# Kernel optimization log

Hardware: AMD Instinct MI355X
Metric: run time of the kernel (lower is better)

The kernel has to match this reference:

```python
import jax, jax.numpy as jnp
import numpy as np
import math

B, N, DIM, H, DH = 4, 1024, 512, 8, 64
INNER = H * DH
TEMP = 0.1
REG_LAMBDA = 0.3
LARGE_NEG = -1.0e9


def setup_inputs() -> dict:
    key = jax.random.key(0)
    ks = jax.random.split(key, 10)
    x = jax.random.normal(ks[0], (B, N, DIM), dtype=jnp.float32)
    # binary channel mask with guaranteed self-connection on the diagonal
    m = jax.random.randint(ks[1], (B, N, N), 0, 2, dtype=jnp.int32)
    eye_i = jnp.eye(N, dtype=jnp.int32)[None]
    attn_mask = jnp.maximum(m, eye_i)
    s = 0.02
    Wq = jax.random.normal(ks[2], (DIM, INNER), dtype=jnp.float32) * s
    bq = jnp.zeros((INNER,), dtype=jnp.float32)
    Wk = jax.random.normal(ks[3], (DIM, INNER), dtype=jnp.float32) * s
    bk = jnp.zeros((INNER,), dtype=jnp.float32)
    Wv = jax.random.normal(ks[4], (DIM, INNER), dtype=jnp.float32) * s
    bv = jnp.zeros((INNER,), dtype=jnp.float32)
    Wo = jax.random.normal(ks[5], (INNER, DIM), dtype=jnpp_dummy()) * s if False else jax.random.normal(ks[5], (INNER, DIM), dtype=jnp.float32) * s
    bo = jnp.zeros((DIM,), dtype=jnp.float32)
    return {"x": x, "attn_mask": attn_mask, "Wq": Wq, "bq": bq, "Wk": Wk,
            "bk": bk, "Wv": Wv, "bv": bv, "Wo": Wo, "bo": bo}


def jnp_dummy():
    return jnp.float32


def _split_heads(t):
    # [b, n, h*d] -> [b, h, n, d]
    return t.reshape(t.shape[0], t.shape[1], H, DH).transpose(0, 2, 1, 3)


def _dynamical_contrastive_loss(scores, attn_mask_f, norm_matrix):
    # cosine similarity matrix (scores / |q||k|)
    cos = scores / norm_matrix
    e = jnp.exp(cos / TEMP)                                   # [b,h,n,n]
    pos = (e * attn_mask_f[:, None]).sum(-1)                  # [b,h,n]
    allsum = e.sum(-1)                                        # [b,h,n]
    clustering = -jnp.log(pos / allsum)
    eye = jnp.eye(N, dtype=attn_mask_f.dtype)
    regular = jnp.abs(attn_mask_f - eye[None]).sum((-2, -1)) / (N * (N - 1))
    return clustering.mean() + REG_LAMBDA * regular.mean()


def reference(x, attn_mask, Wq, bq, Wk, bk, Wv, bv, Wo, bo):
    q = _split_heads(x @ Wq + bq)  # [b,h,n,d]
    k = _split_heads(x @ Wk + bk)
    v = _split_heads(x @ Wv + bv)
    scale = 1.0 / math.sqrt(DH)

    scores = jnp.einsum('bhid,bhjd->bhij', q, k)
    q_norm = jnp.linalg.norm(q, axis=-1, keepdims=True)       # [b,h,n,1]
    k_norm = jnp.linalg.norm(k, axis=-1, keepdims=True)
    norm_matrix = q_norm * jnp.swapaxes(k_norm, -1, -2)       # [b,h,n,n]

    am = attn_mask.astype(scores.dtype)[:, None]              # [b,1,n,n]
    masked_scores = scores * am + (1.0 - am) * LARGE_NEG
    # faithful replication of the all-blocked-row special case
    # (-1e9 is finite so this is a no-op unless scores contain -inf)
    row_all_blocked = jnp.all(jnp.isneginf(masked_scores), axis=-1, keepdims=True)
    masked_scores = jnp.where(row_all_blocked, jnp.zeros_like(masked_scores), masked_scores)

    dcl = _dynamical_contrastive_loss(scores, attn_mask.astype(scores.dtype), norm_matrix)

    attn = jax.nn.softmax(masked_scores * scale, axis=-1)
    out = jnp.einsum('bhij,bhjd->bhid', attn, v)
    out = out.transpose(0, 2, 1, 3).reshape(x.shape[0], x.shape[1], INNER)
    # dropout is identity in eval mode
    return out @ Wo + bo, attn, dcl
```

## Files before the change

### kernel.cpp

```cpp
#include <hip/hip_runtime.h>
#include <hip/hip_bf16.h>
#include <math.h>

#define BB 4
#define NTOK 1024
#define DIMD 512
#define HH 8
#define DH 64
#define INNER 512
#define BH (BB*HH)
#define ROWS (BB*NTOK)
#define SCALE 0.125f
#define INV_TEMP 10.0f

typedef __bf16 bf16_t;
using bf16x4 = __attribute__((ext_vector_type(4))) __bf16;
using bf16x8 = __attribute__((ext_vector_type(8))) __bf16;
using f32x4  = __attribute__((ext_vector_type(4))) float;

__device__ __forceinline__ int swz(int row, int e) { return e ^ ((row & 7) << 3); }

__device__ __forceinline__ void gload_lds16(const bf16_t* g, bf16_t* l)
{
    __builtin_amdgcn_global_load_lds(
        (const __attribute__((address_space(1))) void*)g,
        (__attribute__((address_space(3))) void*)l, 16, 0, 0);
}

template<int TM, int TN, int MT, int NT>
__device__ __forceinline__ void gemm_core(
    const bf16_t* __restrict__ A, int ldA,
    const bf16_t* __restrict__ B, int ldB, int K,
    bf16_t* As, bf16_t* Bs, f32x4 (&acc)[MT][NT])
{
    const int t = threadIdx.x;
    const int w = t >> 6, l = t & 63;
    constexpr int WGN = TN / (NT * 16);
    const int wm = w / WGN, wn = w % WGN;
    const int lrow = l & 15, lk = (l >> 4) * 8;

    for (int k0 = 0; k0 < K; k0 += 32) {
        #pragma unroll
        for (int it = 0; it < TM / 64; ++it) {
            int r = (t >> 2) + it * 64;
            gload_lds16(&A[(size_t)r * ldA + k0 + (t & 3) * 8],
                        As + ((size_t)it * 256 + w * 64) * 8);
        }
        #pragma unroll
        for (int it = 0; it < TN / 64; ++it) {
            int r = (t >> 2) + it * 64;
            gload_lds16(&B[(size_t)r * ldB + k0 + (t & 3) * 8],
                        Bs + ((size_t)it * 256 + w * 64) * 8);
        }
        __syncthreads();
        bf16x8 af[MT], bf[NT];
        #pragma unroll
        for (int mt = 0; mt < MT; ++mt)
            af[mt] = *(const bf16x8*)&As[(wm * MT * 16 + mt * 16 + lrow) * 32 + lk];
        #pragma unroll
        for (int nt = 0; nt < NT; ++nt)
            bf[nt] = *(const bf16x8*)&Bs[(wn * NT * 16 + nt * 16 + lrow) * 32 + lk];
        #pragma unroll
        for (int mt = 0; mt < MT; ++mt)
            #pragma unroll
            for (int nt = 0; nt < NT; ++nt)
                acc[mt][nt] = __builtin_amdgcn_mfma_f32_16x16x32_bf16(
                    af[mt], bf[nt], acc[mt][nt], 0, 0, 0);
        __syncthreads();
    }
}

__global__ __launch_bounds__(256) void prep_kernel(
    const float* __restrict__ x,
    const float* __restrict__ Wq, const float* __restrict__ Wk,
    const float* __restrict__ Wv, const float* __restrict__ Wo,
    const int* __restrict__ mask,
    bf16_t* __restrict__ xb, bf16_t* __restrict__ wt,
    unsigned int* __restrict__ mp)
{
    __shared__ float tile[32][33];
    const int bid = blockIdx.x, t = threadIdx.x;
    if (bid < 2048) {
        int idx = bid * 256 + t;
        float4 v = ((const float4*)x)[idx];
        bf16x4 o = { (bf16_t)v.x, (bf16_t)v.y, (bf16_t)v.z, (bf16_t)v.w };
        ((bf16x4*)xb)[idx] = o;
    } else if (bid < 3072) {
        int f = bid - 2048;
        int bx = f & 15, by = (f >> 4) & 15, z = f >> 8;
        const float* src = (z == 0) ? Wq : (z == 1) ? Wk : (z == 2) ? Wv : Wo;
        bf16_t* dst = wt + (size_t)z * DIMD * INNER;
        const int tx = t & 31, ty = t >> 5;
        const int rBase = by * 32, cBase = bx * 32;
        #pragma unroll
        for (int i = 0; i < 4; ++i)
            tile[ty + i * 8][tx] = src[(size_t)(rBase + ty + i * 8) * INNER + cBase + tx];
        __syncthreads();
        #pragma unroll
        for (int i = 0; i < 4; ++i)
            dst[(size_t)(cBase + ty + i * 8) * DIMD + rBase + tx] = (bf16_t)tile[tx][ty + i * 8];
    } else {
        int f = bid - 3072;
        int rr = f & 255, b = f >> 8;
        const int* mb = mask + ((size_t)(b * NTOK + rr * 4)) * NTOK;
        #pragma unroll
        for (int u = 0; u < 4; ++u) {
            int col = u * 256 + t;
            unsigned int o = (unsigned)mb[col]
                           | ((unsigned)mb[NTOK + col] << 8)
                           | ((unsigned)mb[2 * NTOK + col] << 16)
                           | ((unsigned)mb[3 * NTOK + col] << 24);
            mp[((size_t)b * 256 + rr) * NTOK + col] = o;
        }
    }
}

__global__ __launch_bounds__(256) void qkv_gemm(
    const bf16_t* __restrict__ xb, const bf16_t* __restrict__ wt,
    const float* __restrict__ bq, const float* __restrict__ bk,
    const float* __restrict__ bv,
    bf16_t* __restrict__ qb, bf16_t* __restrict__ kb, bf16_t* __restrict__ vt,
    float* __restrict__ iqn, float* __restrict__ ikn)
{
    __shared__ __align__(16) bf16_t As[128 * 32];
    __shared__ __align__(16) bf16_t Bs[128 * 32];
    const int z = blockIdx.z;
    const bf16_t* Bp = wt + (size_t)z * DIMD * INNER;
    const float* bias = (z == 0) ? bq : (z == 1) ? bk : bv;
    const int rowBase = blockIdx.y * 128, colBase = blockIdx.x * 128;

    f32x4 acc[4][4] = {};
    gemm_core<128, 128, 4, 4>(xb + (size_t)rowBase * DIMD, DIMD,
                              Bp + (size_t)colBase * DIMD, DIMD, DIMD,
                              As, Bs, acc);

    const int l = threadIdx.x & 63, w = threadIdx.x >> 6;
    const int wm = w >> 1, wn = w & 1;
    float nsum[4][4] = {};
    #pragma unroll
    for (int mt = 0; mt < 4; ++mt)
        #pragma unroll
        for (int nt = 0; nt < 4; ++nt)
            #pragma unroll
            for (int r = 0; r < 4; ++r) {
                int grow = rowBase + wm * 64 + mt * 16 + (l >> 4) * 4 + r;
                int gcol = colBase + wn * 64 + nt * 16 + (l & 15);
                float val = acc[mt][nt][r] + bias[gcol];
                bf16_t vb16 = (bf16_t)val;
                int b = grow >> 10, n = grow & 1023, h = gcol >> 6, d = gcol & 63;
                if (z == 0)
                    qb[(((size_t)b * HH + h) * NTOK + n) * DH + d] = vb16;
                else if (z == 1)
                    kb[(((size_t)b * HH + h) * NTOK + n) * DH + d] = vb16;
                else
                    vt[(((size_t)b * HH + h) * DH + d) * NTOK + n] = vb16;
                if (z < 2) { float vb = (float)vb16; nsum[mt][r] += vb * vb; }
            }
    if (z < 2) {
        float* dst = (z == 0) ? iqn : ikn;
        const int h = (colBase >> 6) + wn;
        #pragma unroll
        for (int mt = 0; mt < 4; ++mt)
            #pragma unroll
            for (int r = 0; r < 4; ++r) {
                float s = nsum[mt][r];
                s += __shfl_xor(s, 8); s += __shfl_xor(s, 4);
                s += __shfl_xor(s, 2); s += __shfl_xor(s, 1);
                if ((l & 15) == 0) {
                    int grow = rowBase + wm * 64 + mt * 16 + (l >> 4) * 4 + r;
                    int b = grow >> 10, n = grow & 1023;
                    dst[((size_t)b * HH + h) * NTOK + n] = 1.0f / sqrtf(s);
                }
            }
    }
}

__device__ __forceinline__ void stage_k(const bf16_t* K, int col0, bf16_t* Ks, int t)
{
    const int w = t >> 6, l = t & 63;
    #pragma unroll
    for (int u = 0; u < 4; ++u) {
        int g = u * 256 + w * 64 + l;
        int kr = g >> 3, ep = (g & 7) * 8;
        gload_lds16(K + (size_t)(col0 + kr) * DH + (ep ^ ((kr & 7) << 3)),
                    Ks + ((size_t)u * 256 + w * 64) * 8);
    }
}
__device__ __forceinline__ void stage_v(const bf16_t* V, int col0, bf16_t* Vs, int t)
{
    const int w = t >> 6, l = t & 63;
    #pragma unroll
    for (int u = 0; u < 4; ++u) {
        int g = u * 256 + w * 64 + l;
        int d = g >> 4, ep = (g & 15) * 8;
        gload_lds16(V + (size_t)d * NTOK + col0 + (ep ^ ((d & 7) << 3)),
                    Vs + ((size_t)u * 256 + w * 64) * 8);
    }
}

__global__ __launch_bounds__(256) void attn_fused(
    const bf16_t* __restrict__ qb, const bf16_t* __restrict__ kb,
    const bf16_t* __restrict__ vt, const unsigned int* __restrict__ mp,
    const float* __restrict__ iqn, const float* __restrict__ ikn,
    float* __restrict__ attnf, bf16_t* __restrict__ ctxb,
    float* __restrict__ cl, float* __restrict__ rg)
{
    __shared__ __align__(16) bf16_t Ks[128 * 64];
    __shared__ __align__(16) bf16_t Vs[64 * 128];
    __shared__ __align__(16) bf16_t Ps[4 * 16 * 128];
    const int bh = blockIdx.y;
    const int b = bh >> 3, h = bh & 7;
    const int rowBase = blockIdx.x * 64;
    const bf16_t* Q = qb + (size_t)bh * NTOK * DH;
    const bf16_t* K = kb + (size_t)bh * NTOK * DH;
    const bf16_t* V = vt + (size_t)bh * DH * NTOK;
    const float* iknr = ikn + (size_t)bh * NTOK;
    const int t = threadIdx.x, w = t >> 6, l = t & 63;
    const int l15 = l & 15, q = l >> 4;
    bf16_t* Pw = Ps + w * (16 * 128);

    bf16x8 af[2];
    {
        const bf16_t* qrow = Q + (size_t)(rowBase + w * 16 + l15) * DH + q * 8;
        af[0] = *(const bf16x8*)(qrow);
        af[1] = *(const bf16x8*)(qrow + 32);
    }
    const int tok = rowBase + w * 16 + q * 4;
    float iqn4[4];
    #pragma unroll
    for (int r = 0; r < 4; ++r)
        iqn4[r] = iqn[(size_t)bh * NTOK + tok + r];
    const unsigned int* mrow = mp + ((size_t)b * 256 + (tok >> 2)) * NTOK;

    float alls[4] = {}, pos[4] = {}, esum[4] = {}, regf[4] = {};

    for (int ct = 0; ct < 8; ++ct) {
        const int col0 = ct * 128;
        stage_k(K, col0, Ks, t);
        __syncthreads();
        f32x4 sacc[8] = {};
        #pragma unroll
        for (int ks = 0; ks < 2; ++ks) {
            int koff = ks * 32 + q * 8;
            #pragma unroll
            for (int nt = 0; nt < 8; ++nt) {
                int kr = nt * 16 + l15;
                bf16x8 bfk = *(const bf16x8*)&Ks[kr * 64 + swz(kr, koff)];
                sacc[nt] = __builtin_amdgcn_mfma_f32_16x16x32_bf16(af[ks], bfk, sacc[nt], 0, 0, 0);
            }
        }
        #pragma unroll
        for (int nt = 0; nt < 8; ++nt) {
            int c = col0 + nt * 16 + l15;
            float ik = iknr[c];
            unsigned int mm = mrow[c];
            #pragma unroll
            for (int r = 0; r < 4; ++r) {
                float s = sacc[nt][r];
                float mbit = (float)((mm >> (8 * r)) & 1u);
                float e1 = __expf(s * iqn4[r] * ik * INV_TEMP);
                float e2 = __expf(s * SCALE);
                alls[r] += e1;
                pos[r]  += e1 * mbit;
                esum[r] += e2 * mbit;
                regf[r] += mbit;
            }
        }
        __syncthreads();
    }
    float inv4[4];
    #pragma unroll
    for (int r = 0; r < 4; ++r) {
        #pragma unroll
        for (int off = 8; off; off >>= 1) {
            alls[r] += __shfl_xor(alls[r], off);
            pos[r]  += __shfl_xor(pos[r], off);
            esum[r] += __shfl_xor(esum[r], off);
            regf[r] += __shfl_xor(regf[r], off);
        }
        inv4[r] = 1.0f / esum[r];
    }
    if (l15 == 0) {
        #pragma unroll
        for (int r = 0; r < 4; ++r) {
            int rowG = bh * NTOK + tok + r;
            cl[rowG] = logf(alls[r]) - logf(pos[r]);
            if (h == 0) rg[b * NTOK + tok + r] = regf[r] - 1.0f;
        }
    }

    float* prow = attnf + ((size_t)bh * NTOK + tok) * NTOK;
    f32x4 cacc[4] = {};
    for (int ct = 0; ct < 8; ++ct) {
        const int col0 = ct * 128;
        stage_k(K, col0, Ks, t);
        stage_v(V, col0, Vs, t);
        __syncthreads();
        f32x4 sacc[8] = {};
        #pragma unroll
        for (int ks = 0; ks < 2; ++ks) {
            int koff = ks * 32 + q * 8;
            #pragma unroll
            for (int nt = 0; nt < 8; ++nt) {
                int kr = nt * 16 + l15;
                bf16x8 bfk = *(const bf16x8*)&Ks[kr * 64 + swz(kr, koff)];
                sacc[nt] = __builtin_amdgcn_mfma_f32_16x16x32_bf16(af[ks], bfk, sacc[nt], 0, 0, 0);
            }
        }
        #pragma unroll
        for (int nt = 0; nt < 8; ++nt) {
            int c = nt * 16 + l15;
            unsigned int mm = mrow[col0 + c];
            #pragma unroll
            for (int r = 0; r < 4; ++r) {
                float p = ((mm >> (8 * r)) & 1u)
                        ? __expf(sacc[nt][r] * SCALE) * inv4[r] : 0.0f;
                prow[(size_t)r * NTOK + col0 + c] = p;
                int pr = q * 4 + r;
                Pw[pr * 128 + swz(pr, c)] = (bf16_t)p;
            }
        }
        #pragma unroll
        for (int ks = 0; ks < 4; ++ks) {
            int koff = ks * 32 + q * 8;
            bf16x8 afp = *(const bf16x8*)&Pw[l15 * 128 + swz(l15, koff)];
            #pragma unroll
            for (int nt = 0; nt < 4; ++nt) {
                int d = nt * 16 + l15;
                bf16x8 bfv = *(const bf16x8*)&Vs[d * 128 + swz(d, koff)];
                cacc[nt] = __builtin_amdgcn_mfma_f32_16x16x32_bf16(afp, bfv, cacc[nt], 0, 0, 0);
            }
        }
        __syncthreads();
    }
    #pragma unroll
    for (int nt = 0; nt < 4; ++nt)
        #pragma unroll
        for (int r = 0; r < 4; ++r) {
            int n = tok + r;
            int d = nt * 16 + l15;
            ctxb[((size_t)b * NTOK + n) * INNER + h * DH + d] = (bf16_t)cacc[nt][r];
        }
}

__device__ __forceinline__ float block_sum(float v, float* sh)
{
    #pragma unroll
    for (int off = 32; off; off >>= 1) v += __shfl_down(v, off);
    __syncthreads();
    if ((threadIdx.x & 63) == 0) sh[threadIdx.x >> 6] = v;
    __syncthreads();
    return sh[0] + sh[1] + sh[2] + sh[3];
}

__global__ __launch_bounds__(256) void out_gemm(
    const bf16_t* __restrict__ ctxb, const bf16_t* __restrict__ wt,
    const float* __restrict__ bo, float* __restrict__ outp,
    const float* __restrict__ cl, const float* __restrict__ rg,
    float* __restrict__ dcl)
{
    __shared__ __align__(16) bf16_t As[128 * 32];
    __shared__ __align__(16) bf16_t Bs[128 * 32];
    __shared__ float sh4[4];
    const int rowBase = blockIdx.y * 128, colBase = blockIdx.x * 128;
    const bf16_t* Wot = wt + (size_t)3 * DIMD * INNER;

    f32x4 acc[4][4] = {};
    gemm_core<128, 128, 4, 4>(ctxb + (size_t)rowBase * INNER, INNER,
                              Wot + (size_t)colBase * INNER, INNER, INNER,
                              As, Bs, acc);

    const int l = threadIdx.x & 63, w = threadIdx.x >> 6;
    const int wm = w >> 1, wn = w & 1;
    #pragma unroll
    for (int mt = 0; mt < 4; ++mt)
        #pragma unroll
        for (int nt = 0; nt < 4; ++nt)
            #pragma unroll
            for (int r = 0; r < 4; ++r) {
                int grow = rowBase + wm * 64 + mt * 16 + (l >> 4) * 4 + r;
                int gcol = colBase + wn * 64 + nt * 16 + (l & 15);
                outp[(size_t)grow * DIMD + gcol] = acc[mt][nt][r] + bo[gcol];
            }

    if (blockIdx.x == 0 && blockIdx.y == 0) {
        float s1 = 0.f, s2 = 0.f;
        for (int idx = threadIdx.x; idx < BH * NTOK; idx += 256) s1 += cl[idx];
        for (int idx = threadIdx.x; idx < BB * NTOK; idx += 256) s2 += rg[idx];
        __syncthreads();
        s1 = block_sum(s1, sh4);
        s2 = block_sum(s2, sh4);
        if (threadIdx.x == 0) {
            dcl[0] = s1 * (1.0f / (float)(BB * HH * NTOK))
                   + 0.3f * s2 * (1.0f / ((float)NTOK * (float)(NTOK - 1) * (float)BB));
        }
    }
}

extern "C" void kernel_launch(void* const* d_in, const int* in_sizes, int n_in,
                              void* d_out, int out_size, void* d_ws, size_t ws_size,
                              hipStream_t stream)
{
    const float* x  = (const float*)d_in[0];
    const int* mask = (const int*)d_in[1];
    const float* Wq = (const float*)d_in[2];
    const float* bq = (const float*)d_in[3];
    const float* Wk = (const float*)d_in[4];
    const float* bk = (const float*)d_in[5];
    const float* Wv = (const float*)d_in[6];
    const float* bv = (const float*)d_in[7];
    const float* Wo = (const float*)d_in[8];
    const float* bo = (const float*)d_in[9];

    float* out   = (float*)d_out;
    float* attnf = out + (size_t)ROWS * DIMD;
    float* dcl   = attnf + (size_t)BH * NTOK * NTOK;

    char* wsb = (char*)d_ws;
    bf16_t* xb    = (bf16_t*)wsb;
    bf16_t* wt    = xb + (size_t)ROWS * DIMD;
    bf16_t* qb    = wt + (size_t)4 * DIMD * INNER;
    bf16_t* kb    = qb + (size_t)BH * NTOK * DH;
    bf16_t* vt    = kb + (size_t)BH * NTOK * DH;
    bf16_t* ctxb  = vt + (size_t)BH * NTOK * DH;
    float*  iqn   = (float*)(ctxb + (size_t)ROWS * INNER);
    float*  ikn   = iqn + BH * NTOK;
    float*  cl    = ikn + BH * NTOK;
    float*  rg    = cl + BH * NTOK;
    unsigned int* mpk = (unsigned int*)(rg + BB * NTOK);

    dim3 blk(256);
    prep_kernel<<<dim3(4096), blk, 0, stream>>>(x, Wq, Wk, Wv, Wo, mask, xb, wt, mpk);
    qkv_gemm<<<dim3(4, 32, 3), blk, 0, stream>>>(xb, wt, bq, bk, bv, qb, kb, vt, iqn, ikn);
    attn_fused<<<dim3(16, 32), blk, 0, stream>>>(qb, kb, vt, mpk, iqn, ikn, attnf, ctxb, cl, rg);
    out_gemm<<<dim3(4, 32), blk, 0, stream>>>(ctxb, wt, bo, out, cl, rg, dcl);
}
```

Baseline: 289.8 us.

## Split attention key range across two wave groups with 512-thread blocks

Measured after the change: 274.6 us. -5.3%, faster.

```diff
diff --git a/kernel.cpp b/kernel.cpp
--- a/kernel.cpp
+++ b/kernel.cpp
@@ -175,39 +175,17 @@
     }
 }
 
-__device__ __forceinline__ void stage_k(const bf16_t* K, int col0, bf16_t* Ks, int t)
-{
-    const int w = t >> 6, l = t & 63;
-    #pragma unroll
-    for (int u = 0; u < 4; ++u) {
-        int g = u * 256 + w * 64 + l;
-        int kr = g >> 3, ep = (g & 7) * 8;
-        gload_lds16(K + (size_t)(col0 + kr) * DH + (ep ^ ((kr & 7) << 3)),
-                    Ks + ((size_t)u * 256 + w * 64) * 8);
-    }
-}
-__device__ __forceinline__ void stage_v(const bf16_t* V, int col0, bf16_t* Vs, int t)
-{
-    const int w = t >> 6, l = t & 63;
-    #pragma unroll
-    for (int u = 0; u < 4; ++u) {
-        int g = u * 256 + w * 64 + l;
-        int d = g >> 4, ep = (g & 15) * 8;
-        gload_lds16(V + (size_t)d * NTOK + col0 + (ep ^ ((d & 7) << 3)),
-                    Vs + ((size_t)u * 256 + w * 64) * 8);
-    }
-}
-
-__global__ __launch_bounds__(256) void attn_fused(
+__global__ __launch_bounds__(512) void attn_fused(
     const bf16_t* __restrict__ qb, const bf16_t* __restrict__ kb,
     const bf16_t* __restrict__ vt, const unsigned int* __restrict__ mp,
     const float* __restrict__ iqn, const float* __restrict__ ikn,
     float* __restrict__ attnf, bf16_t* __restrict__ ctxb,
     float* __restrict__ cl, float* __restrict__ rg)
 {
-    __shared__ __align__(16) bf16_t Ks[128 * 64];
-    __shared__ __align__(16) bf16_t Vs[64 * 128];
-    __shared__ __align__(16) bf16_t Ps[4 * 16 * 128];
+    __shared__ __align__(16) bf16_t Ks[2][64 * 64];
+    __shared__ __align__(16) bf16_t Vs[2][64 * 64];
+    __shared__ __align__(16) bf16_t Ps[8][16 * 64];
+    __shared__ float4 sred[8][16];
     const int bh = blockIdx.y;
     const int b = bh >> 3, h = bh & 7;
     const int rowBase = blockIdx.x * 64;
@@ -216,16 +194,17 @@
     const bf16_t* V = vt + (size_t)bh * DH * NTOK;
     const float* iknr = ikn + (size_t)bh * NTOK;
     const int t = threadIdx.x, w = t >> 6, l = t & 63;
+    const int half = w >> 2, rw = w & 3;
     const int l15 = l & 15, q = l >> 4;
-    bf16_t* Pw = Ps + w * (16 * 128);
+    bf16_t* Pw = Ps[w];
 
     bf16x8 af[2];
     {
-        const bf16_t* qrow = Q + (size_t)(rowBase + w * 16 + l15) * DH + q * 8;
+        const bf16_t* qrow = Q + (size_t)(rowBase + rw * 16 + l15) * DH + q * 8;
         af[0] = *(const bf16x8*)(qrow);
         af[1] = *(const bf16x8*)(qrow + 32);
     }
-    const int tok = rowBase + w * 16 + q * 4;
+    const int tok = rowBase + rw * 16 + q * 4;
     float iqn4[4];
     #pragma unroll
     for (int r = 0; r < 4; ++r)
@@ -234,26 +213,38 @@
 
     float alls[4] = {}, pos[4] = {}, esum[4] = {}, regf[4] = {};
 
-    for (int ct = 0; ct < 8; ++ct) {
-        const int col0 = ct * 128;
-        stage_k(K, col0, Ks, t);
-        __syncthreads();
-        f32x4 sacc[8] = {};
+    for (int tt = 0; tt < 8; ++tt) {
+        const int col0 = half * 512 + tt * 64;
+        #pragma unroll
+        for (int u = 0; u < 2; ++u) {
+            int g = (u * 8 + w) * 64 + l;
+            int hh = g >> 9, kr = (g >> 3) & 63, ci = g & 7;
+            gload_lds16(K + (size_t)(hh * 512 + tt * 64 + kr) * DH + ((ci * 8) ^ ((kr & 7) << 3)),
+                        &Ks[0][0] + (size_t)(u * 8 + w) * 512);
+        }
+        unsigned int mm4[4]; float ik4[4];
+        #pragma unroll
+        for (int nt = 0; nt < 4; ++nt) {
+            int c = col0 + nt * 16 + l15;
+            mm4[nt] = mrow[c];
+            ik4[nt] = iknr[c];
+        }
+        __syncthreads();
+        f32x4 sacc[4] = {};
         #pragma unroll
         for (int ks = 0; ks < 2; ++ks) {
             int koff = ks * 32 + q * 8;
             #pragma unroll
-            for (int nt = 0; nt < 8; ++nt) {
+            for (int nt = 0; nt < 4; ++nt) {
                 int kr = nt * 16 + l15;
-                bf16x8 bfk = *(const bf16x8*)&Ks[kr * 64 + swz(kr, koff)];
+                bf16x8 bfk = *(const bf16x8*)&Ks[half][kr * 64 + swz(kr, koff)];
                 sacc[nt] = __builtin_amdgcn_mfma_f32_16x16x32_bf16(af[ks], bfk, sacc[nt], 0, 0, 0);
             }
         }
         #pragma unroll
-        for (int nt = 0; nt < 8; ++nt) {
-            int c = col0 + nt * 16 + l15;
-            float ik = iknr[c];
-            unsigned int mm = mrow[c];
+        for (int nt = 0; nt < 4; ++nt) {
+            float ik = ik4[nt];
+            unsigned int mm = mm4[nt];
             #pragma unroll
             for (int r = 0; r < 4; ++r) {
                 float s = sacc[nt][r];
@@ -268,7 +259,6 @@
         }
         __syncthreads();
     }
-    float inv4[4];
     #pragma unroll
     for (int r = 0; r < 4; ++r) {
         #pragma unroll
@@ -278,69 +268,109 @@
             esum[r] += __shfl_xor(esum[r], off);
             regf[r] += __shfl_xor(regf[r], off);
         }
-        inv4[r] = 1.0f / esum[r];
     }
     if (l15 == 0) {
         #pragma unroll
-        for (int r = 0; r < 4; ++r) {
+        for (int r = 0; r < 4; ++r)
+            sred[w][q * 4 + r] = make_float4(alls[r], pos[r], esum[r], regf[r]);
+    }
+    __syncthreads();
+    float inv4[4];
+    #pragma unroll
+    for (int r = 0; r < 4; ++r) {
+        float4 o = sred[w ^ 4][q * 4 + r];
+        float allsT = alls[r] + o.x;
+        float posT  = pos[r]  + o.y;
+        float esumT = esum[r] + o.z;
+        float regT  = regf[r] + o.w;
+        inv4[r] = 1.0f / esumT;
+        if (half == 0 && l15 == 0) {
             int rowG = bh * NTOK + tok + r;
-            cl[rowG] = logf(alls[r]) - logf(pos[r]);
-            if (h == 0) rg[b * NTOK + tok + r] = regf[r] - 1.0f;
+            cl[rowG] = logf(allsT) - logf(posT);
+            if (h == 0) rg[b * NTOK + tok + r] = regT - 1.0f;
         }
     }
 
     float* prow = attnf + ((size_t)bh * NTOK + tok) * NTOK;
     f32x4 cacc[4] = {};
-    for (int ct = 0; ct < 8; ++ct) {
-        const int col0 = ct * 128;
-        stage_k(K, col0, Ks, t);
-        stage_v(V, col0, Vs, t);
-        __syncthreads();
-        f32x4 sacc[8] = {};
+    for (int tt = 0; tt < 8; ++tt) {
+        const int col0 = half * 512 + tt * 64;
+        #pragma unroll
+        for (int u = 0; u < 2; ++u) {
+            int g = (u * 8 + w) * 64 + l;
+            int hh = g >> 9, kr = (g >> 3) & 63, ci = g & 7;
+            gload_lds16(K + (size_t)(hh * 512 + tt * 64 + kr) * DH + ((ci * 8) ^ ((kr & 7) << 3)),
+                        &Ks[0][0] + (size_t)(u * 8 + w) * 512);
+        }
+        #pragma unroll
+        for (int u = 0; u < 2; ++u) {
+            int g = (u * 8 + w) * 64 + l;
+            int hh = g >> 9, d = (g >> 3) & 63, ci = g & 7;
+            gload_lds16(V + (size_t)d * NTOK + hh * 512 + tt * 64 + (((ci * 8)) ^ ((d & 7) << 3)),
+                        &Vs[0][0] + (size_t)(u * 8 + w) * 512);
+        }
+        unsigned int mm4[4];
+        #pragma unroll
+        for (int nt = 0; nt < 4; ++nt)
+            mm4[nt] = mrow[col0 + nt * 16 + l15];
+        __syncthreads();
+        f32x4 sacc[4] = {};
         #pragma unroll
         for (int ks = 0; ks < 2; ++ks) {
             int koff = ks * 32 + q * 8;
             #pragma unroll
-            for (int nt = 0; nt < 8; ++nt) {
+            for (int nt = 0; nt < 4; ++nt) {
                 int kr = nt * 16 + l15;
-                bf16x8 bfk = *(const bf16x8*)&Ks[kr * 64 + swz(kr, koff)];
+                bf16x8 bfk = *(const bf16x8*)&Ks[half][kr * 64 + swz(kr, koff)];
                 sacc[nt] = __builtin_amdgcn_mfma_f32_16x16x32_bf16(af[ks], bfk, sacc[nt], 0, 0, 0);
             }
         }
         #pragma unroll
-        for (int nt = 0; nt < 8; ++nt) {
+        for (int nt = 0; nt < 4; ++nt) {
             int c = nt * 16 + l15;
-            unsigned int mm = mrow[col0 + c];
+            unsigned int mm = mm4[nt];
             #pragma unroll
             for (int r = 0; r < 4; ++r) {
                 float p = ((mm >> (8 * r)) & 1u)
                         ? __expf(sacc[nt][r] * SCALE) * inv4[r] : 0.0f;
                 prow[(size_t)r * NTOK + col0 + c] = p;
                 int pr = q * 4 + r;
-                Pw[pr * 128 + swz(pr, c)] = (bf16_t)p;
-            }
-        }
-        #pragma unroll
-        for (int ks = 0; ks < 4; ++ks) {
+                Pw[pr * 64 + swz(pr, c)] = (bf16_t)p;
+            }
+        }
+        #pragma unroll
+        for (int ks = 0; ks < 2; ++ks) {
             int koff = ks * 32 + q * 8;
-            bf16x8 afp = *(const bf16x8*)&Pw[l15 * 128 + swz(l15, koff)];
+            bf16x8 afp = *(const bf16x8*)&Pw[l15 * 64 + swz(l15, koff)];
             #pragma unroll
             for (int nt = 0; nt < 4; ++nt) {
                 int d = nt * 16 + l15;
-                bf16x8 bfv = *(const bf16x8*)&Vs[d * 128 + swz(d, koff)];
+                bf16x8 bfv = *(const bf16x8*)&Vs[half][d * 64 + swz(d, koff)];
                 cacc[nt] = __builtin_amdgcn_mfma_f32_16x16x32_bf16(afp, bfv, cacc[nt], 0, 0, 0);
             }
         }
         __syncthreads();
     }
-    #pragma unroll
-    for (int nt = 0; nt < 4; ++nt)
-        #pragma unroll
-        for (int r = 0; r < 4; ++r) {
-            int n = tok + r;
-            int d = nt * 16 + l15;
-            ctxb[((size_t)b * NTOK + n) * INNER + h * DH + d] = (bf16_t)cacc[nt][r];
-        }
+    float* cred = (float*)&Ps[0][0];
+    if (half == 1) {
+        #pragma unroll
+        for (int nt = 0; nt < 4; ++nt)
+            #pragma unroll
+            for (int r = 0; r < 4; ++r)
+                cred[(size_t)rw * 1024 + (q * 4 + r) * 64 + nt * 16 + l15] = cacc[nt][r];
+    }
+    __syncthreads();
+    if (half == 0) {
+        #pragma unroll
+        for (int nt = 0; nt < 4; ++nt)
+            #pragma unroll
+            for (int r = 0; r < 4; ++r) {
+                float v = cacc[nt][r] + cred[(size_t)rw * 1024 + (q * 4 + r) * 64 + nt * 16 + l15];
+                int n = tok + r;
+                int d = nt * 16 + l15;
+                ctxb[((size_t)b * NTOK + n) * INNER + h * DH + d] = (bf16_t)v;
+            }
+    }
 }
 
 __device__ __forceinline__ float block_sum(float v, float* sh)
@@ -432,6 +462,6 @@
     dim3 blk(256);
     prep_kernel<<<dim3(4096), blk, 0, stream>>>(x, Wq, Wk, Wv, Wo, mask, xb, wt, mpk);
     qkv_gemm<<<dim3(4, 32, 3), blk, 0, stream>>>(xb, wt, bq, bk, bv, qb, kb, vt, iqn, ikn);
-    attn_fused<<<dim3(16, 32), blk, 0, stream>>>(qb, kb, vt, mpk, iqn, ikn, attnf, ctxb, cl, rg);
+    attn_fused<<<dim3(16, 32), dim3(512), 0, stream>>>(qb, kb, vt, mpk, iqn, ikn, attnf, ctxb, cl, rg);
     out_gemm<<<dim3(4, 32), blk, 0, stream>>>(ctxb, wt, bo, out, cl, rg, dcl);
 }
```
